# Performance work log

Hardware: AMD Instinct MI355X
Metric: run time of the kernel (lower is better)

## Reference

```python
import jax, jax.numpy as jnp
import numpy as np
from functools import partial

# Module hyperparameters (from init_kwargs)
T, C_IN, H, W_DIM = 128, 16, 64, 64
C_OUT, KH, KW = 64, 3, 3
PAD = ((1, 1), (1, 1))  # (top,bottom),(left,right) -> symmetric here
STRIDES = (1, 1)
F_V_THRESH = 8.0
F_V_THRESH_LOW = -1.0
F_V_RESET = 0.0
# fVSubtract is None -> reset-to-value branch


def setup_inputs() -> dict:
    key = jax.random.key(0)
    kx, kw, kb = jax.random.split(key, 3)
    x = jax.random.uniform(kx, (T, C_IN, H, W_DIM), dtype=jnp.float32)
    fan_in = C_IN * KH * KW
    bound = 1.0 / np.sqrt(fan_in)
    W = jax.random.uniform(kw, (C_OUT, C_IN, KH, KW), dtype=jnp.float32,
                           minval=-bound, maxval=bound)
    b = jax.random.uniform(kb, (C_OUT,), dtype=jnp.float32,
                           minval=-bound, maxval=bound)
    return {"x": x, "W": W, "b": b}


def _spiking_conv(x, W, b):
    # conv over all timesteps at once (time is the conv batch dim): [T, C_out, H, W]
    conv_out = jax.lax.conv_general_dilated(
        x, W, window_strides=STRIDES, padding=PAD,
        dimension_numbers=("NCHW", "OIHW", "NCHW"))
    conv_out = conv_out + b[None, :, None, None]

    def step(state, conv_t):
        state = state + conv_t
        spikes = (state >= F_V_THRESH).astype(conv_t.dtype)
        # reset-to-value branch (fVSubtract is None)
        state = spikes * F_V_RESET + state * (1.0 - spikes)
        # nn.Threshold(v, v): x if x > v else v
        state = jnp.where(state > F_V_THRESH_LOW, state, F_V_THRESH_LOW)
        return state, spikes

    init_state = jnp.zeros(conv_out.shape[1:], dtype=conv_out.dtype)
    _, num_spikes = jax.lax.scan(step, init_state, conv_out)
    return num_spikes  # [T, C_out, H, W] float (0/1)


def reference(x, W, b):
    return _spiking_conv(x, W, b)
```

## Files before the change

kernel.cpp:

```cpp
#include <hip/hip_runtime.h>

#define T_STEPS 128
#define CIN     16
#define HH      64
#define WW      64
#define COUT    64
#define HWSZ    (HH * WW)
#define CHW     (COUT * HWSZ)
#define XCHW    (CIN * HWSZ)

#define TILE    32
#define HALO    34
#define LSTR    36
#define PLANE   (HALO * LSTR)
#define NST     (CIN * HALO * HALO)
#define WBLK    80

__global__ void transpose_w(const float* __restrict__ W, float* __restrict__ Wtr) {
    int e = blockIdx.x * 256 + threadIdx.x;
    if (e >= COUT * CIN * 9) return;
    int co = e / (CIN * 9);
    int r  = e - co * (CIN * 9);
    int ci = r / 9;
    int k  = r - ci * 9;
    int coq = co >> 4, cog = (co >> 3) & 1, j = co & 7;
    Wtr[(((coq * 2 + cog) * CIN) + ci) * WBLK + j * 9 + k] = W[e];
}

__global__ __launch_bounds__(512, 4)
void spiking_conv_pass1(const float* __restrict__ x, const float* __restrict__ Wtr,
                        const float* __restrict__ b, float* __restrict__ out) {
    __shared__ float xs[CIN * PLANE];

    const int tid = threadIdx.x;
    const int t   = blockIdx.y;
    const int h0  = (blockIdx.x >> 1) * TILE;
    const int w0  = (blockIdx.x & 1) * TILE;
    const int coq = blockIdx.z;

    const float* xt = x + t * XCHW;
    for (int e = tid; e < NST; e += 512) {
        int ci  = e / (HALO * HALO);
        int rem = e - ci * (HALO * HALO);
        int r   = rem / HALO;
        int c   = rem - r * HALO;
        int gh  = h0 - 1 + r;
        int gw  = w0 - 1 + c;
        float v = 0.f;
        if ((unsigned)gh < HH && (unsigned)gw < WW)
            v = xt[ci * HWSZ + gh * WW + gw];
        xs[ci * PLANE + r * LSTR + c] = v;
    }
    __syncthreads();

    const int cog = __builtin_amdgcn_readfirstlane(tid >> 8);
    const int sp  = tid & 255;
    const int pr0 = sp >> 3;
    const int pc0 = (sp & 7) * 4;
    const float* wbase = Wtr + (coq * 2 + cog) * (CIN * WBLK);
    float* outt = out + t * CHW;

    float acc[8][4];
#pragma unroll
    for (int j = 0; j < 8; ++j)
#pragma unroll
        for (int p = 0; p < 4; ++p) acc[j][p] = 0.f;

#pragma unroll 1
    for (int ci = 0; ci < CIN; ++ci) {
        float xv[3][6];
#pragma unroll
        for (int dr = 0; dr < 3; ++dr) {
            const float* row = &xs[ci * PLANE + (pr0 + dr) * LSTR + pc0];
            float4 a  = *(const float4*)row;
            float2 c2 = *(const float2*)(row + 4);
            xv[dr][0] = a.x;  xv[dr][1] = a.y;
            xv[dr][2] = a.z;  xv[dr][3] = a.w;
            xv[dr][4] = c2.x; xv[dr][5] = c2.y;
        }
#pragma unroll
        for (int half = 0; half < 2; ++half) {
            float w[36];
#pragma unroll
            for (int i = 0; i < 36; ++i)
                w[i] = wbase[ci * WBLK + half * 36 + i];
#pragma unroll
            for (int jj = 0; jj < 4; ++jj) {
                const int j = half * 4 + jj;
#pragma unroll
                for (int ky = 0; ky < 3; ++ky)
#pragma unroll
                    for (int kx = 0; kx < 3; ++kx) {
                        const float wv = w[jj * 9 + ky * 3 + kx];
#pragma unroll
                        for (int p = 0; p < 4; ++p)
                            acc[j][p] += wv * xv[ky][kx + p];
                    }
            }
        }
    }

#pragma unroll
    for (int j = 0; j < 8; ++j) {
        const int co = coq * 16 + cog * 8 + j;
        const float bias = b[co];
        float4 o;
        o.x = acc[j][0] + bias;
        o.y = acc[j][1] + bias;
        o.z = acc[j][2] + bias;
        o.w = acc[j][3] + bias;
        *(float4*)&outt[co * HWSZ + (h0 + pr0) * WW + (w0 + pc0)] = o;
    }
}

__global__ __launch_bounds__(256)
void spiking_scan_pass2(float* __restrict__ io) {
    const int idx = blockIdx.x * 256 + threadIdx.x;
    float* p = io + idx;
    float s = 0.f;
    float v[16], nv[16];
#pragma unroll
    for (int i = 0; i < 16; ++i) v[i] = p[i * CHW];
#pragma unroll 1
    for (int tb = 0; tb < 7; ++tb) {
#pragma unroll
        for (int i = 0; i < 16; ++i) nv[i] = p[((tb + 1) * 16 + i) * CHW];
        float o[16];
#pragma unroll
        for (int i = 0; i < 16; ++i) {
            s += v[i];
            const bool sp = (s >= 8.0f);
            o[i] = sp ? 1.0f : 0.0f;
            s = sp ? 0.0f : s;
            s = fmaxf(s, -1.0f);
        }
#pragma unroll
        for (int i = 0; i < 16; ++i) p[(tb * 16 + i) * CHW] = o[i];
#pragma unroll
        for (int i = 0; i < 16; ++i) v[i] = nv[i];
    }
#pragma unroll
    for (int i = 0; i < 16; ++i) {
        s += v[i];
        const bool sp = (s >= 8.0f);
        p[(112 + i) * CHW] = sp ? 1.0f : 0.0f;
        s = sp ? 0.0f : s;
        s = fmaxf(s, -1.0f);
    }
}

extern "C" void kernel_launch(void* const* d_in, const int* in_sizes, int n_in,
                              void* d_out, int out_size, void* d_ws, size_t ws_size,
                              hipStream_t stream) {
    const float* x = (const float*)d_in[0];
    const float* W = (const float*)d_in[1];
    const float* b = (const float*)d_in[2];
    float* out = (float*)d_out;
    float* Wtr = (float*)d_ws;

    transpose_w<<<36, 256, 0, stream>>>(W, Wtr);

    dim3 g1(4, 128, 4);
    spiking_conv_pass1<<<g1, 512, 0, stream>>>(x, Wtr, b, out);

    spiking_scan_pass2<<<CHW / 256, 256, 0, stream>>>(out);
}
```

Before: 309.1 us.

## Double output channels per thread, batch halo loads, vectorize scan with float4

Each conv block now computes 32 output channels (16 per thread) instead of 16, halving the number of blocks and the redundant loading of the input halo tile. The halo staging loop is unrolled so all global loads are issued before the shared-memory stores, giving more memory-level parallelism. The scan pass processes four pixels per thread with float4 loads and stores and a quarter of the threads. The doubled accumulator count raises register pressure under the 512x4 launch bound and may cause spills or lower occupancy, and the smaller scan grid gives less parallelism.

```diff
diff --git a/kernel.cpp b/kernel.cpp
--- a/kernel.cpp
+++ b/kernel.cpp
@@ -14,7 +14,7 @@
 #define LSTR    36
 #define PLANE   (HALO * LSTR)
 #define NST     (CIN * HALO * HALO)
-#define WBLK    80
+#define WBLK    40
 
 __global__ void transpose_w(const float* __restrict__ W, float* __restrict__ Wtr) {
     int e = blockIdx.x * 256 + threadIdx.x;
@@ -23,8 +23,7 @@
     int r  = e - co * (CIN * 9);
     int ci = r / 9;
     int k  = r - ci * 9;
-    int coq = co >> 4, cog = (co >> 3) & 1, j = co & 7;
-    Wtr[(((coq * 2 + cog) * CIN) + ci) * WBLK + j * 9 + k] = W[e];
+    Wtr[((co >> 2) * CIN + ci) * WBLK + (co & 3) * 9 + k] = W[e];
 }
 
 __global__ __launch_bounds__(512, 4)
@@ -36,20 +35,42 @@
     const int t   = blockIdx.y;
     const int h0  = (blockIdx.x >> 1) * TILE;
     const int w0  = (blockIdx.x & 1) * TILE;
-    const int coq = blockIdx.z;
+    const int coh = blockIdx.z;
 
     const float* xt = x + t * XCHW;
-    for (int e = tid; e < NST; e += 512) {
-        int ci  = e / (HALO * HALO);
-        int rem = e - ci * (HALO * HALO);
-        int r   = rem / HALO;
-        int c   = rem - r * HALO;
-        int gh  = h0 - 1 + r;
-        int gw  = w0 - 1 + c;
-        float v = 0.f;
-        if ((unsigned)gh < HH && (unsigned)gw < WW)
-            v = xt[ci * HWSZ + gh * WW + gw];
-        xs[ci * PLANE + r * LSTR + c] = v;
+    {
+        float vbuf[19]; int ibuf[19];
+#pragma unroll
+        for (int k = 0; k < 18; ++k) {
+            unsigned e = tid + k * 512;
+            unsigned ci = e / (HALO * HALO);
+            unsigned rem = e - ci * (HALO * HALO);
+            unsigned r  = rem / HALO;
+            unsigned c  = rem - r * HALO;
+            int gh = h0 - 1 + (int)r;
+            int gw = w0 - 1 + (int)c;
+            bool inb = (unsigned)gh < HH && (unsigned)gw < WW;
+            vbuf[k] = inb ? xt[ci * HWSZ + gh * WW + gw] : 0.f;
+            ibuf[k] = ci * PLANE + r * LSTR + c;
+        }
+#pragma unroll
+        for (int k = 0; k < 18; ++k) xs[ibuf[k]] = vbuf[k];
+#pragma unroll
+        for (int k = 0; k < 19; ++k) {
+            unsigned e = tid + (18 + k) * 512;
+            unsigned ci = e / (HALO * HALO);
+            unsigned rem = e - ci * (HALO * HALO);
+            unsigned r  = rem / HALO;
+            unsigned c  = rem - r * HALO;
+            int gh = h0 - 1 + (int)r;
+            int gw = w0 - 1 + (int)c;
+            bool inb = e < NST && (unsigned)gh < HH && (unsigned)gw < WW;
+            vbuf[k] = inb ? xt[ci * HWSZ + gh * WW + gw] : 0.f;
+            ibuf[k] = (e < NST) ? (int)(ci * PLANE + r * LSTR + c) : -1;
+        }
+#pragma unroll
+        for (int k = 0; k < 19; ++k)
+            if (ibuf[k] >= 0) xs[ibuf[k]] = vbuf[k];
     }
     __syncthreads();
 
@@ -57,12 +78,11 @@
     const int sp  = tid & 255;
     const int pr0 = sp >> 3;
     const int pc0 = (sp & 7) * 4;
-    const float* wbase = Wtr + (coq * 2 + cog) * (CIN * WBLK);
     float* outt = out + t * CHW;
 
-    float acc[8][4];
+    float acc[16][4];
 #pragma unroll
-    for (int j = 0; j < 8; ++j)
+    for (int j = 0; j < 16; ++j)
 #pragma unroll
         for (int p = 0; p < 4; ++p) acc[j][p] = 0.f;
 
@@ -79,14 +99,14 @@
             xv[dr][4] = c2.x; xv[dr][5] = c2.y;
         }
 #pragma unroll
-        for (int half = 0; half < 2; ++half) {
+        for (int g = 0; g < 4; ++g) {
+            const int g4 = coh * 8 + cog * 4 + g;
+            const float* wb = Wtr + (g4 * CIN + ci) * WBLK;
             float w[36];
 #pragma unroll
-            for (int i = 0; i < 36; ++i)
-                w[i] = wbase[ci * WBLK + half * 36 + i];
+            for (int i = 0; i < 36; ++i) w[i] = wb[i];
 #pragma unroll
-            for (int jj = 0; jj < 4; ++jj) {
-                const int j = half * 4 + jj;
+            for (int jj = 0; jj < 4; ++jj)
 #pragma unroll
                 for (int ky = 0; ky < 3; ++ky)
 #pragma unroll
@@ -94,58 +114,58 @@
                         const float wv = w[jj * 9 + ky * 3 + kx];
 #pragma unroll
                         for (int p = 0; p < 4; ++p)
-                            acc[j][p] += wv * xv[ky][kx + p];
+                            acc[g * 4 + jj][p] += wv * xv[ky][kx + p];
                     }
-            }
         }
     }
 
 #pragma unroll
-    for (int j = 0; j < 8; ++j) {
-        const int co = coq * 16 + cog * 8 + j;
-        const float bias = b[co];
-        float4 o;
-        o.x = acc[j][0] + bias;
-        o.y = acc[j][1] + bias;
-        o.z = acc[j][2] + bias;
-        o.w = acc[j][3] + bias;
-        *(float4*)&outt[co * HWSZ + (h0 + pr0) * WW + (w0 + pc0)] = o;
-    }
+    for (int g = 0; g < 4; ++g)
+#pragma unroll
+        for (int jj = 0; jj < 4; ++jj) {
+            const int co = coh * 32 + cog * 16 + g * 4 + jj;
+            const float bias = b[co];
+            float4 o;
+            o.x = acc[g * 4 + jj][0] + bias;
+            o.y = acc[g * 4 + jj][1] + bias;
+            o.z = acc[g * 4 + jj][2] + bias;
+            o.w = acc[g * 4 + jj][3] + bias;
+            *(float4*)&outt[co * HWSZ + (h0 + pr0) * WW + (w0 + pc0)] = o;
+        }
 }
 
 __global__ __launch_bounds__(256)
 void spiking_scan_pass2(float* __restrict__ io) {
     const int idx = blockIdx.x * 256 + threadIdx.x;
-    float* p = io + idx;
-    float s = 0.f;
-    float v[16], nv[16];
+    float4* p = (float4*)io + idx;
+    float sx = 0.f, sy = 0.f, sz = 0.f, sw = 0.f;
+    float4 v[8], nv[8];
 #pragma unroll
-    for (int i = 0; i < 16; ++i) v[i] = p[i * CHW];
+    for (int i = 0; i < 8; ++i) v[i] = p[(size_t)i * (CHW / 4)];
 #pragma unroll 1
-    for (int tb = 0; tb < 7; ++tb) {
+    for (int tb = 0; tb < 15; ++tb) {
 #pragma unroll
-        for (int i = 0; i < 16; ++i) nv[i] = p[((tb + 1) * 16 + i) * CHW];
-        float o[16];
+        for (int i = 0; i < 8; ++i) nv[i] = p[(size_t)((tb + 1) * 8 + i) * (CHW / 4)];
 #pragma unroll
-        for (int i = 0; i < 16; ++i) {
-            s += v[i];
-            const bool sp = (s >= 8.0f);
-            o[i] = sp ? 1.0f : 0.0f;
-            s = sp ? 0.0f : s;
-            s = fmaxf(s, -1.0f);
+        for (int i = 0; i < 8; ++i) {
+            float4 o;
+            sx += v[i].x; bool a0 = (sx >= 8.0f); o.x = a0 ? 1.f : 0.f; sx = a0 ? 0.f : sx; sx = fmaxf(sx, -1.f);
+            sy += v[i].y; bool a1 = (sy >= 8.0f); o.y = a1 ? 1.f : 0.f; sy = a1 ? 0.f : sy; sy = fmaxf(sy, -1.f);
+            sz += v[i].z; bool a2 = (sz >= 8.0f); o.z = a2 ? 1.f : 0.f; sz = a2 ? 0.f : sz; sz = fmaxf(sz, -1.f);
+            sw += v[i].w; bool a3 = (sw >= 8.0f); o.w = a3 ? 1.f : 0.f; sw = a3 ? 0.f : sw; sw = fmaxf(sw, -1.f);
+            p[(size_t)(tb * 8 + i) * (CHW / 4)] = o;
         }
 #pragma unroll
-        for (int i = 0; i < 16; ++i) p[(tb * 16 + i) * CHW] = o[i];
-#pragma unroll
-        for (int i = 0; i < 16; ++i) v[i] = nv[i];
+        for (int i = 0; i < 8; ++i) v[i] = nv[i];
     }
 #pragma unroll
-    for (int i = 0; i < 16; ++i) {
-        s += v[i];
-        const bool sp = (s >= 8.0f);
-        p[(112 + i) * CHW] = sp ? 1.0f : 0.0f;
-        s = sp ? 0.0f : s;
-        s = fmaxf(s, -1.0f);
+    for (int i = 0; i < 8; ++i) {
+        float4 o;
+        sx += v[i].x; bool a0 = (sx >= 8.0f); o.x = a0 ? 1.f : 0.f; sx = a0 ? 0.f : sx; sx = fmaxf(sx, -1.f);
+        sy += v[i].y; bool a1 = (sy >= 8.0f); o.y = a1 ? 1.f : 0.f; sy = a1 ? 0.f : sy; sy = fmaxf(sy, -1.f);
+        sz += v[i].z; bool a2 = (sz >= 8.0f); o.z = a2 ? 1.f : 0.f; sz = a2 ? 0.f : sz; sz = fmaxf(sz, -1.f);
+        sw += v[i].w; bool a3 = (sw >= 8.0f); o.w = a3 ? 1.f : 0.f; sw = a3 ? 0.f : sw; sw = fmaxf(sw, -1.f);
+        p[(size_t)(120 + i) * (CHW / 4)] = o;
     }
 }
 
@@ -160,8 +180,8 @@
 
     transpose_w<<<36, 256, 0, stream>>>(W, Wtr);
 
-    dim3 g1(4, 128, 4);
+    dim3 g1(4, 128, 2);
     spiking_conv_pass1<<<g1, 512, 0, stream>>>(x, Wtr, b, out);
 
-    spiking_scan_pass2<<<CHW / 256, 256, 0, stream>>>(out);
+    spiking_scan_pass2<<<(CHW / 4) / 256, 256, 0, stream>>>(out);
 }
```

Result: faster. 263.9 us (-14.6%).
